# Kernel tuning notes

Measured on AMD Instinct MI355X. Metric: run time of the kernel, lower is better.

## Reference

```python
import jax, jax.numpy as jnp
import numpy as np

B, S, H = 16, 1024, 256
NH = 4
DH = H // NH


def setup_inputs() -> dict:
    key = jax.random.key(0)
    ks = jax.random.split(key, 12)
    w = lambda i, shape: jax.random.normal(ks[i], shape, dtype=jnp.float32) * 0.02
    return {
        "step_sequence": jax.random.normal(ks[0], (B, S, H), dtype=jnp.float32),
        "final_outcomes": jax.random.normal(ks[1], (B,), dtype=jnp.float32),
        "step_mask": jnp.ones((B, S), dtype=jnp.bool_),
        # MultiheadAttention q/k projections (only attn weights are used)
        "Wq": w(2, (H, H)), "bq": jnp.zeros((H,), jnp.float32),
        "Wk": w(3, (H, H)), "bk": jnp.zeros((H,), jnp.float32),
        # causal_mask_predictor: Linear(H,H//2)-ReLU-Linear(H//2,1)-Sigmoid
        "Wm1": w(4, (H, H // 2)), "bm1": jnp.zeros((H // 2,), jnp.float32),
        "Wm2": w(5, (H // 2, 1)), "bm2": jnp.zeros((1,), jnp.float32),
        # intervention_generator: Linear(H,H)-ReLU-Linear(H,H)-Tanh
        "Wi1": w(6, (H, H)), "bi1": jnp.zeros((H,), jnp.float32),
        "Wi2": w(7, (H, H)), "bi2": jnp.zeros((H,), jnp.float32),
        # credit_estimator: Linear(H,H//2)-ReLU-Linear(H//2,1)
        "We1": w(8, (H, H // 2)), "be1": jnp.zeros((H // 2,), jnp.float32),
        "We2": w(9, (H // 2, 1)), "be2": jnp.zeros((1,), jnp.float32),
    }


def _forward(x, final_outcomes, step_mask, Wq, bq, Wk, bk, Wm1, bm1, Wm2, bm2,
             Wi1, bi1, Wi2, bi2, We1, be1, We2, be2):
    # --- CausalAttentionModule ---
    q = (x @ Wq + bq).reshape(B, S, NH, DH).transpose(0, 2, 1, 3)  # [B,NH,S,DH]
    k = (x @ Wk + bk).reshape(B, S, NH, DH).transpose(0, 2, 1, 3)
    scores = jnp.einsum('bhqd,bhkd->bhqk', q, k) / jnp.sqrt(jnp.float32(DH))
    scores = jnp.where(step_mask[:, None, None, :], scores, -jnp.inf)  # key_padding_mask
    attn = jax.nn.softmax(scores, axis=-1).mean(axis=1)  # head-averaged [B,S,S]
    strengths = jax.nn.sigmoid(jax.nn.relu(x @ Wm1 + bm1) @ Wm2 + bm2)[..., 0]  # [B,S]
    aw_mean = attn.mean(axis=1)  # mean over query dim -> [B,S]
    cm = aw_mean[:, None, :] * strengths[:, :, None]  # [B,S,S]
    cm = cm * jnp.tril(jnp.ones((S, S), dtype=x.dtype))[None]
    # --- interventional credit (vectorized over the B x S python loop) ---
    colmean = cm.mean(axis=1)  # mean_i cm[b,i,j] -> [B,S]
    base = (x * colmean[..., None]).mean(axis=1)  # [B,H] baseline weighted-mean feature
    # intervention changes only row t: delta = 0.1*tanh-MLP(x_t)
    delta = 0.1 * jnp.tanh(jax.nn.relu(x @ Wi1 + bi1) @ Wi2 + bi2)  # [B,S,H]
    feats = base[:, None, :] + delta * colmean[..., None] / S  # [B,S,H]
    outcomes = (jax.nn.relu(feats @ We1 + be1) @ We2 + be2)[..., 0]  # [B,S]
    credit = jnp.where(step_mask, final_outcomes[:, None] - outcomes, 0.0)
    return credit, cm


def reference(step_sequence, final_outcomes, step_mask, Wq, bq, Wk, bk,
              Wm1, bm1, Wm2, bm2, Wi1, bi1, Wi2, bi2, We1, be1, We2, be2):
    return _forward(step_sequence, final_outcomes, step_mask, Wq, bq, Wk, bk,
                    Wm1, bm1, Wm2, bm2, Wi1, bi1, Wi2, bi2, We1, be1, We2, be2)
```

## Files before the change

kernel.cpp:

```cpp
#include <hip/hip_runtime.h>
#include <hip/hip_bf16.h>
#include <math.h>

#define B 16
#define S 1024
#define H 256
#define NH 4
#define DH 64
#define BS (B*S)
#define XSTR 264
#define L2E 1.4426950408889634f

typedef short short8 __attribute__((ext_vector_type(8)));
typedef float f32x16 __attribute__((ext_vector_type(16)));

__device__ __forceinline__ unsigned short to_bf16(float v) {
  __hip_bfloat16 h = __float2bfloat16(v);
  return *(unsigned short*)&h;
}
__device__ __forceinline__ unsigned int pack_bf16x2(float a, float b) {
  return (unsigned int)to_bf16(a) | ((unsigned int)to_bf16(b) << 16);
}
__device__ __forceinline__ float exp2_hw(float v) {
  return __builtin_amdgcn_exp2f(v);
}

__global__ __launch_bounds__(256) void k_convert_w(
    const float* __restrict__ Wq, const float* __restrict__ Wk,
    const float* __restrict__ Wm1, const float* __restrict__ Wi1,
    const float* __restrict__ Wi2, const float* __restrict__ We1,
    unsigned short* __restrict__ WqT, unsigned short* __restrict__ WkT,
    unsigned short* __restrict__ Wm1T, unsigned short* __restrict__ Wi1T,
    unsigned short* __restrict__ Wi2T, unsigned short* __restrict__ We1T)
{
  const float* src; unsigned short* dst; int N;
  switch (blockIdx.y) {
    case 0: src = Wq;  dst = WqT;  N = 256; break;
    case 1: src = Wk;  dst = WkT;  N = 256; break;
    case 2: src = Wm1; dst = Wm1T; N = 128; break;
    case 3: src = Wi1; dst = Wi1T; N = 256; break;
    case 4: src = Wi2; dst = Wi2T; N = 256; break;
    default: src = We1; dst = We1T; N = 128; break;
  }
  int ntiles = N >> 5;
  int tile = blockIdx.x;
  if (tile >= 8 * ntiles) return;
  int kt = tile / ntiles, nt = tile % ntiles;
  __shared__ float tl[32][33];
  int t = threadIdx.x, r = t >> 5, c = t & 31;
  #pragma unroll
  for (int i = 0; i < 4; ++i)
    tl[r + i*8][c] = src[(kt*32 + r + i*8)*N + nt*32 + c];
  __syncthreads();
  #pragma unroll
  for (int i = 0; i < 4; ++i)
    dst[(nt*32 + r + i*8)*256 + kt*32 + c] = to_bf16(tl[c][r + i*8]);
}

__global__ __launch_bounds__(256) void k_qkproj_mfma(
    const float* __restrict__ x,
    const unsigned short* __restrict__ WqT, const unsigned short* __restrict__ WkT,
    const float* __restrict__ bq, const float* __restrict__ bk,
    unsigned short* __restrict__ qbuf, unsigned short* __restrict__ kbuf)
{
  __shared__ unsigned short xs[32*XSTR];
  int t = threadIdx.x, wave = t >> 6, lane = t & 63;
  int l5 = lane & 31, h5 = lane >> 5;
  int r0 = blockIdx.x * 32;
  {
    const float4* xg = (const float4*)(x + (size_t)r0*H);
    #pragma unroll
    for (int it = 0; it < 8; ++it) {
      int u = it*256 + t, r = u >> 6, c4 = u & 63;
      float4 v = xg[u];
      uint2 pk; pk.x = pack_bf16x2(v.x, v.y); pk.y = pack_bf16x2(v.z, v.w);
      *(uint2*)&xs[r*XSTR + c4*4] = pk;
    }
  }
  __syncthreads();
  int n0 = wave*64 + l5;
  f32x16 aq0, aq1, ak0, ak1;
  #pragma unroll
  for (int r = 0; r < 16; ++r) { aq0[r]=0.f; aq1[r]=0.f; ak0[r]=0.f; ak1[r]=0.f; }
  #pragma unroll 8
  for (int kc = 0; kc < 16; ++kc) {
    short8 a  = *(const short8*)&xs[l5*XSTR + kc*16 + h5*8];
    short8 q0 = *(const short8*)&WqT[(size_t)n0*256 + kc*16 + h5*8];
    short8 q1 = *(const short8*)&WqT[(size_t)(n0+32)*256 + kc*16 + h5*8];
    short8 k0 = *(const short8*)&WkT[(size_t)n0*256 + kc*16 + h5*8];
    short8 k1 = *(const short8*)&WkT[(size_t)(n0+32)*256 + kc*16 + h5*8];
    aq0 = __builtin_amdgcn_mfma_f32_32x32x16_bf16(a, q0, aq0, 0, 0, 0);
    aq1 = __builtin_amdgcn_mfma_f32_32x32x16_bf16(a, q1, aq1, 0, 0, 0);
    ak0 = __builtin_amdgcn_mfma_f32_32x32x16_bf16(a, k0, ak0, 0, 0, 0);
    ak1 = __builtin_amdgcn_mfma_f32_32x32x16_bf16(a, k1, ak1, 0, 0, 0);
  }
  const float qsc = 0.125f * L2E;
  __syncthreads();
  {
    float b0 = bq[n0], b1 = bq[n0+32];
    #pragma unroll
    for (int r = 0; r < 16; ++r) {
      int row = (r & 3) + 8*(r >> 2) + 4*h5;
      xs[row*XSTR + n0]      = to_bf16((aq0[r] + b0) * qsc);
      xs[row*XSTR + n0 + 32] = to_bf16((aq1[r] + b1) * qsc);
    }
  }
  __syncthreads();
  #pragma unroll
  for (int it = 0; it < 4; ++it) {
    int u = it*256 + t, r = u >> 5, c8 = u & 31;
    int mg = r0 + r, bb = mg >> 10, s = mg & 1023;
    int hh = c8 >> 3, dd = (c8 & 7) * 8;
    *(uint4*)&qbuf[(size_t)(((bb*NH + hh)*S + s)*DH + dd)] = *(uint4*)&xs[r*XSTR + c8*8];
  }
  __syncthreads();
  {
    float b0 = bk[n0], b1 = bk[n0+32];
    #pragma unroll
    for (int r = 0; r < 16; ++r) {
      int row = (r & 3) + 8*(r >> 2) + 4*h5;
      xs[row*XSTR + n0]      = to_bf16(ak0[r] + b0);
      xs[row*XSTR + n0 + 32] = to_bf16(ak1[r] + b1);
    }
  }
  __syncthreads();
  #pragma unroll
  for (int it = 0; it < 4; ++it) {
    int u = it*256 + t, r = u >> 5, c8 = u & 31;
    int mg = r0 + r, bb = mg >> 10, s = mg & 1023;
    int hh = c8 >> 3, dd = (c8 & 7) * 8;
    *(uint4*)&kbuf[(size_t)(((bb*NH + hh)*S + s)*DH + dd)] = *(uint4*)&xs[r*XSTR + c8*8];
  }
}

__global__ __launch_bounds__(256) void k_strengths_mfma(
    const float* __restrict__ x, const unsigned short* __restrict__ Wm1T,
    const float* __restrict__ bm1, const float* __restrict__ Wm2, const float* __restrict__ bm2,
    float* __restrict__ strengths)
{
  __shared__ unsigned short xs[32*XSTR];
  __shared__ float red[4][32];
  int t = threadIdx.x, wave = t >> 6, lane = t & 63;
  int l5 = lane & 31, h5 = lane >> 5;
  int r0 = blockIdx.x * 32;
  {
    const float4* xg = (const float4*)(x + (size_t)r0*H);
    #pragma unroll
    for (int it = 0; it < 8; ++it) {
      int u = it*256 + t, r = u >> 6, c4 = u & 63;
      float4 v = xg[u];
      uint2 pk; pk.x = pack_bf16x2(v.x, v.y); pk.y = pack_bf16x2(v.z, v.w);
      *(uint2*)&xs[r*XSTR + c4*4] = pk;
    }
  }
  __syncthreads();
  f32x16 acc;
  #pragma unroll
  for (int r = 0; r < 16; ++r) acc[r] = 0.f;
  int n = wave*32 + l5;
  #pragma unroll 8
  for (int kc = 0; kc < 16; ++kc) {
    short8 a = *(const short8*)&xs[l5*XSTR + kc*16 + h5*8];
    short8 b = *(const short8*)&Wm1T[(size_t)n*256 + kc*16 + h5*8];
    acc = __builtin_amdgcn_mfma_f32_32x32x16_bf16(a, b, acc, 0, 0, 0);
  }
  float bi = bm1[n], w2 = Wm2[n];
  #pragma unroll
  for (int r = 0; r < 16; ++r) {
    float v = fmaxf(acc[r] + bi, 0.f) * w2;
    #pragma unroll
    for (int off = 1; off <= 16; off <<= 1) v += __shfl_xor(v, off);
    if (l5 == 0) red[wave][(r & 3) + 8*(r >> 2) + 4*h5] = v;
  }
  __syncthreads();
  if (t < 32) {
    float s = red[0][t] + red[1][t] + red[2][t] + red[3][t] + bm2[0];
    strengths[r0 + t] = 1.f / (1.f + __expf(-s));
  }
}

__global__ __launch_bounds__(256) void k_attn_mfma(
    const unsigned short* __restrict__ qbuf, const unsigned short* __restrict__ kbuf,
    float* __restrict__ aw_part)
{
  __shared__ float part[4][64];
  int t = threadIdx.x, wave = t >> 6, lane = t & 63;
  int l5 = lane & 31, h5 = lane >> 5;
  int qt = blockIdx.x, i0 = qt * 64;
  int h = blockIdx.y, b = blockIdx.z;
  const unsigned short* qg = qbuf + (size_t)((b*NH + h)*S + i0) * DH;
  const unsigned short* kg = kbuf + (size_t)((b*NH + h)*S) * DH;

  short8 af[2][4];
  #pragma unroll
  for (int rt = 0; rt < 2; ++rt)
    #pragma unroll
    for (int kc = 0; kc < 4; ++kc)
      af[rt][kc] = *(const short8*)(qg + (rt*32 + l5)*DH + kc*16 + h5*8);

  float lacc[2][16];
  #pragma unroll
  for (int rt = 0; rt < 2; ++rt)
    #pragma unroll
    for (int r = 0; r < 16; ++r) lacc[rt][r] = 0.f;

  unsigned int pp[8][2][8];
  #pragma unroll
  for (int kt = 0; kt < 8; ++kt) {
    short8 bfr[4];
    #pragma unroll
    for (int kc = 0; kc < 4; ++kc)
      bfr[kc] = *(const short8*)(kg + (size_t)(kt*128 + wave*32 + l5)*DH + kc*16 + h5*8);
    f32x16 a0, a1;
    #pragma unroll
    for (int r = 0; r < 16; ++r) { a0[r] = 0.f; a1[r] = 0.f; }
    #pragma unroll
    for (int kc = 0; kc < 4; ++kc) {
      a0 = __builtin_amdgcn_mfma_f32_32x32x16_bf16(af[0][kc], bfr[kc], a0, 0, 0, 0);
      a1 = __builtin_amdgcn_mfma_f32_32x32x16_bf16(af[1][kc], bfr[kc], a1, 0, 0, 0);
    }
    #pragma unroll
    for (int r2 = 0; r2 < 8; ++r2) {
      float p0 = exp2_hw(a0[2*r2]), p1 = exp2_hw(a0[2*r2+1]);
      lacc[0][2*r2] += p0; lacc[0][2*r2+1] += p1;
      pp[kt][0][r2] = pack_bf16x2(p0, p1);
      float q0 = exp2_hw(a1[2*r2]), q1 = exp2_hw(a1[2*r2+1]);
      lacc[1][2*r2] += q0; lacc[1][2*r2+1] += q1;
      pp[kt][1][r2] = pack_bf16x2(q0, q1);
    }
  }
  #pragma unroll
  for (int rt = 0; rt < 2; ++rt)
    #pragma unroll
    for (int r = 0; r < 16; ++r) {
      float v = lacc[rt][r];
      #pragma unroll
      for (int off = 1; off <= 16; off <<= 1) v += __shfl_xor(v, off);
      lacc[rt][r] = v;
    }
  if (l5 == 0) {
    #pragma unroll
    for (int rt = 0; rt < 2; ++rt)
      #pragma unroll
      for (int r = 0; r < 16; ++r)
        part[wave][rt*32 + (r & 3) + 8*(r >> 2) + 4*h5] = lacc[rt][r];
  }
  __syncthreads();
  float linv[2][16];
  #pragma unroll
  for (int rt = 0; rt < 2; ++rt)
    #pragma unroll
    for (int r = 0; r < 16; ++r) {
      int row = rt*32 + (r & 3) + 8*(r >> 2) + 4*h5;
      linv[rt][r] = 1.f / (part[0][row] + part[1][row] + part[2][row] + part[3][row]);
    }
  #pragma unroll
  for (int kt = 0; kt < 8; ++kt) {
    float csum = 0.f;
    #pragma unroll
    for (int rt = 0; rt < 2; ++rt)
      #pragma unroll
      for (int r2 = 0; r2 < 8; ++r2) {
        unsigned int u = pp[kt][rt][r2];
        float p0 = __uint_as_float(u << 16);
        float p1 = __uint_as_float(u & 0xffff0000u);
        csum += p0 * linv[rt][2*r2] + p1 * linv[rt][2*r2+1];
      }
    csum += __shfl_xor(csum, 32);
    if (lane < 32)
      aw_part[(size_t)qt*BS + b*S + kt*128 + wave*32 + lane] = csum;
  }
}

__global__ __launch_bounds__(256) void k_colmean(
    const float* __restrict__ strengths, const float* __restrict__ aw_part,
    float* __restrict__ aw_mean, float* __restrict__ colmean)
{
  __shared__ float st[1024];
  int t = threadIdx.x, b = blockIdx.x;
  #pragma unroll
  for (int e = 0; e < 4; ++e) st[t + e*256] = strengths[b*S + t + e*256];
  __syncthreads();
  for (int off = 1; off < 1024; off <<= 1) {
    float tmp[4];
    #pragma unroll
    for (int e = 0; e < 4; ++e) {
      int j = t + e*256;
      tmp[e] = (j + off < 1024) ? st[j + off] : 0.f;
    }
    __syncthreads();
    #pragma unroll
    for (int e = 0; e < 4; ++e) st[t + e*256] += tmp[e];
    __syncthreads();
  }
  #pragma unroll
  for (int e = 0; e < 4; ++e) {
    int j = t + e*256;
    float s = 0.f;
    #pragma unroll
    for (int qt = 0; qt < 16; ++qt) s += aw_part[(size_t)qt*BS + b*S + j];
    float am = s * (1.f / (NH * (float)S));
    aw_mean[b*S + j] = am;
    colmean[b*S + j] = am * st[j] * (1.f / (float)S);
  }
}

__global__ __launch_bounds__(256) void k_cm(
    const float* __restrict__ aw_mean, const float* __restrict__ strengths,
    float* __restrict__ cm_out)
{
  int t = threadIdx.x;
  int row = blockIdx.x;
  int b = row >> 10, i = row & 1023;
  float sti = strengths[row];
  float4 v = ((const float4*)(aw_mean + b*S))[t];
  int j0 = t * 4;
  float4 o;
  o.x = (j0 + 0 <= i) ? v.x * sti : 0.f;
  o.y = (j0 + 1 <= i) ? v.y * sti : 0.f;
  o.z = (j0 + 2 <= i) ? v.z * sti : 0.f;
  o.w = (j0 + 3 <= i) ? v.w * sti : 0.f;
  ((float4*)cm_out)[(size_t)row*(S/4) + t] = o;
}

__global__ __launch_bounds__(256) void k_base(
    const float* __restrict__ x, const float* __restrict__ colmean,
    float* __restrict__ base_part)
{
  int t = threadIdx.x;
  int chunk = blockIdx.x, b = blockIdx.y;
  float acc = 0.f;
  int t0 = chunk * 32;
  for (int tt = 0; tt < 32; ++tt) {
    int srow = t0 + tt;
    acc += x[(size_t)(b*S + srow)*H + t] * colmean[b*S + srow];
  }
  base_part[(size_t)chunk*B*H + b*H + t] = acc * (1.f / (float)S);
}

__global__ __launch_bounds__(256) void k_credit_mfma(
    const float* __restrict__ x, const float* __restrict__ base_part,
    const float* __restrict__ colmean,
    const unsigned short* __restrict__ Wi1T, const float* __restrict__ bi1,
    const unsigned short* __restrict__ Wi2T, const float* __restrict__ bi2,
    const unsigned short* __restrict__ We1T, const float* __restrict__ be1,
    const float* __restrict__ We2, const float* __restrict__ be2,
    const float* __restrict__ final_outcomes, float* __restrict__ credit_out)
{
  __shared__ unsigned short xs[32*XSTR];
  __shared__ unsigned short hs[32*XSTR];
  __shared__ float cmv_s[32];
  __shared__ float red[4][32];
  int t = threadIdx.x, wave = t >> 6, lane = t & 63;
  int l5 = lane & 31, h5 = lane >> 5;
  int r0 = blockIdx.x * 32;
  int b = r0 >> 10;
  {
    const float4* xg = (const float4*)(x + (size_t)r0*H);
    #pragma unroll
    for (int it = 0; it < 8; ++it) {
      int u = it*256 + t, r = u >> 6, c4 = u & 63;
      float4 v = xg[u];
      uint2 pk; pk.x = pack_bf16x2(v.x, v.y); pk.y = pack_bf16x2(v.z, v.w);
      *(uint2*)&xs[r*XSTR + c4*4] = pk;
    }
  }
  if (t < 32) cmv_s[t] = colmean[r0 + t];
  int n0 = wave*64 + l5;
  float bb0 = 0.f, bb1 = 0.f;
  #pragma unroll
  for (int c = 0; c < 32; ++c) {
    bb0 += base_part[(size_t)c*B*H + b*H + n0];
    bb1 += base_part[(size_t)c*B*H + b*H + n0 + 32];
  }
  __syncthreads();

  {
    f32x16 acc0, acc1;
    #pragma unroll
    for (int r = 0; r < 16; ++r) { acc0[r] = 0.f; acc1[r] = 0.f; }
    #pragma unroll 8
    for (int kc = 0; kc < 16; ++kc) {
      short8 a = *(const short8*)&xs[l5*XSTR + kc*16 + h5*8];
      short8 b0 = *(const short8*)&Wi1T[(size_t)n0*256 + kc*16 + h5*8];
      short8 b1 = *(const short8*)&Wi1T[(size_t)(n0+32)*256 + kc*16 + h5*8];
      acc0 = __builtin_amdgcn_mfma_f32_32x32x16_bf16(a, b0, acc0, 0, 0, 0);
      acc1 = __builtin_amdgcn_mfma_f32_32x32x16_bf16(a, b1, acc1, 0, 0, 0);
    }
    float bi0 = bi1[n0], biv1 = bi1[n0 + 32];
    #pragma unroll
    for (int r = 0; r < 16; ++r) {
      int row = (r & 3) + 8*(r >> 2) + 4*h5;
      hs[row*XSTR + n0]      = to_bf16(fmaxf(acc0[r] + bi0, 0.f));
      hs[row*XSTR + n0 + 32] = to_bf16(fmaxf(acc1[r] + biv1, 0.f));
    }
  }
  __syncthreads();
  {
    f32x16 acc0, acc1;
    #pragma unroll
    for (int r = 0; r < 16; ++r) { acc0[r] = 0.f; acc1[r] = 0.f; }
    #pragma unroll 8
    for (int kc = 0; kc < 16; ++kc) {
      short8 a = *(const short8*)&hs[l5*XSTR + kc*16 + h5*8];
      short8 b0 = *(const short8*)&Wi2T[(size_t)n0*256 + kc*16 + h5*8];
      short8 b1 = *(const short8*)&Wi2T[(size_t)(n0+32)*256 + kc*16 + h5*8];
      acc0 = __builtin_amdgcn_mfma_f32_32x32x16_bf16(a, b0, acc0, 0, 0, 0);
      acc1 = __builtin_amdgcn_mfma_f32_32x32x16_bf16(a, b1, acc1, 0, 0, 0);
    }
    float bi0 = bi2[n0], biv1 = bi2[n0 + 32];
    __syncthreads();
    #pragma unroll
    for (int r = 0; r < 16; ++r) {
      int row = (r & 3) + 8*(r >> 2) + 4*h5;
      float cmv = cmv_s[row] * (0.1f / (float)S);
      float e0 = __expf(2.f*(acc0[r] + bi0));
      float e1 = __expf(2.f*(acc1[r] + biv1));
      float th0 = (e0 - 1.f) / (e0 + 1.f);
      float th1 = (e1 - 1.f) / (e1 + 1.f);
      xs[row*XSTR + n0]      = to_bf16(bb0 + th0 * cmv);
      xs[row*XSTR + n0 + 32] = to_bf16(bb1 + th1 * cmv);
    }
  }
  __syncthreads();
  {
    f32x16 acc;
    #pragma unroll
    for (int r = 0; r < 16; ++r) acc[r] = 0.f;
    int n = wave*32 + l5;
    #pragma unroll 8
    for (int kc = 0; kc < 16; ++kc) {
      short8 a = *(const short8*)&xs[l5*XSTR + kc*16 + h5*8];
      short8 bfrag = *(const short8*)&We1T[(size_t)n*256 + kc*16 + h5*8];
      acc = __builtin_amdgcn_mfma_f32_32x32x16_bf16(a, bfrag, acc, 0, 0, 0);
    }
    float bev = be1[n], w2 = We2[n];
    #pragma unroll
    for (int r = 0; r < 16; ++r) {
      float v = fmaxf(acc[r] + bev, 0.f) * w2;
      #pragma unroll
      for (int off = 1; off <= 16; off <<= 1) v += __shfl_xor(v, off);
      if (l5 == 0) red[wave][(r & 3) + 8*(r >> 2) + 4*h5] = v;
    }
  }
  __syncthreads();
  if (t < 32) {
    float s = red[0][t] + red[1][t] + red[2][t] + red[3][t] + be2[0];
    credit_out[r0 + t] = final_outcomes[b] - s;
  }
}

extern "C" void kernel_launch(void* const* d_in, const int* in_sizes, int n_in,
                              void* d_out, int out_size, void* d_ws, size_t ws_size,
                              hipStream_t stream) {
  (void)in_sizes; (void)n_in; (void)out_size; (void)ws_size;
  const float* x   = (const float*)d_in[0];
  const float* fin = (const float*)d_in[1];
  const float* Wq  = (const float*)d_in[3];  const float* bq  = (const float*)d_in[4];
  const float* Wk  = (const float*)d_in[5];  const float* bk  = (const float*)d_in[6];
  const float* Wm1 = (const float*)d_in[7];  const float* bm1 = (const float*)d_in[8];
  const float* Wm2 = (const float*)d_in[9];  const float* bm2 = (const float*)d_in[10];
  const float* Wi1 = (const float*)d_in[11]; const float* bi1 = (const float*)d_in[12];
  const float* Wi2 = (const float*)d_in[13]; const float* bi2 = (const float*)d_in[14];
  const float* We1 = (const float*)d_in[15]; const float* be1 = (const float*)d_in[16];
  const float* We2 = (const float*)d_in[17]; const float* be2 = (const float*)d_in[18];

  unsigned short* us = (unsigned short*)d_ws;
  unsigned short* qb   = us;
  unsigned short* kb   = qb + (size_t)B*NH*S*DH;
  unsigned short* WqT  = kb + (size_t)B*NH*S*DH;
  unsigned short* WkT  = WqT + 65536;
  unsigned short* Wi1T = WkT + 65536;
  unsigned short* Wi2T = Wi1T + 65536;
  unsigned short* Wm1T = Wi2T + 65536;
  unsigned short* We1T = Wm1T + 32768;
  float* fs = (float*)(We1T + 32768);
  float* aw_part   = fs;
  float* strengths = aw_part + 16*BS;
  float* aw_mean   = strengths + BS;
  float* colmean   = aw_mean + BS;
  float* base_part = colmean + BS;

  float* credit_out = (float*)d_out;
  float* cm_out     = credit_out + BS;

  k_convert_w     <<<dim3(64, 6), 256, 0, stream>>>(Wq, Wk, Wm1, Wi1, Wi2, We1,
                                                    WqT, WkT, Wm1T, Wi1T, Wi2T, We1T);
  k_qkproj_mfma   <<<BS/32, 256, 0, stream>>>(x, WqT, WkT, bq, bk, qb, kb);
  k_strengths_mfma<<<BS/32, 256, 0, stream>>>(x, Wm1T, bm1, Wm2, bm2, strengths);
  k_attn_mfma     <<<dim3(S/64, NH, B), 256, 0, stream>>>(qb, kb, aw_part);
  k_colmean       <<<B, 256, 0, stream>>>(strengths, aw_part, aw_mean, colmean);
  k_base          <<<dim3(32, B), 256, 0, stream>>>(x, colmean, base_part);
  k_cm            <<<BS, 256, 0, stream>>>(aw_mean, strengths, cm_out);
  k_credit_mfma   <<<BS/32, 256, 0, stream>>>(x, base_part, colmean, Wi1T, bi1, Wi2T, bi2,
                                              We1T, be1, We2, be2, fin, credit_out);
}
```

Measured before the change: 233.1 us.

## Recompute attention scores in a second pass instead of caching probabilities in registers

The attention kernel now handles 32 query rows per block instead of 64. Rather than keeping every exp-score in a large packed-bf16 register array, it makes two passes over the keys. The first pass accumulates row sums, and the second recomputes QK^T and normalizes with exp2(score - log2(sum)). This frees many registers to raise occupancy and doubles the grid, at the cost of twice the MFMA and K loads. The per-tile partial buffer also doubles, so colmean now sums 32 partials.

After: 250.1 us. 7.3% more time.

```diff
diff --git a/kernel.cpp b/kernel.cpp
--- a/kernel.cpp
+++ b/kernel.cpp
@@ -23,6 +23,9 @@
 }
 __device__ __forceinline__ float exp2_hw(float v) {
   return __builtin_amdgcn_exp2f(v);
+}
+__device__ __forceinline__ float log2_hw(float v) {
+  return __builtin_amdgcn_logf(v);
 }
 
 __global__ __launch_bounds__(256) void k_convert_w(
@@ -183,92 +186,73 @@
     const unsigned short* __restrict__ qbuf, const unsigned short* __restrict__ kbuf,
     float* __restrict__ aw_part)
 {
-  __shared__ float part[4][64];
+  __shared__ float part[4][32];
   int t = threadIdx.x, wave = t >> 6, lane = t & 63;
   int l5 = lane & 31, h5 = lane >> 5;
-  int qt = blockIdx.x, i0 = qt * 64;
+  int qt = blockIdx.x, i0 = qt * 32;
   int h = blockIdx.y, b = blockIdx.z;
   const unsigned short* qg = qbuf + (size_t)((b*NH + h)*S + i0) * DH;
   const unsigned short* kg = kbuf + (size_t)((b*NH + h)*S) * DH;
 
-  short8 af[2][4];
-  #pragma unroll
-  for (int rt = 0; rt < 2; ++rt)
-    #pragma unroll
-    for (int kc = 0; kc < 4; ++kc)
-      af[rt][kc] = *(const short8*)(qg + (rt*32 + l5)*DH + kc*16 + h5*8);
-
-  float lacc[2][16];
-  #pragma unroll
-  for (int rt = 0; rt < 2; ++rt)
-    #pragma unroll
-    for (int r = 0; r < 16; ++r) lacc[rt][r] = 0.f;
-
-  unsigned int pp[8][2][8];
-  #pragma unroll
+  short8 af[4];
+  #pragma unroll
+  for (int kc = 0; kc < 4; ++kc)
+    af[kc] = *(const short8*)(qg + l5*DH + kc*16 + h5*8);
+
+  float lacc[16];
+  #pragma unroll
+  for (int r = 0; r < 16; ++r) lacc[r] = 0.f;
+
   for (int kt = 0; kt < 8; ++kt) {
     short8 bfr[4];
     #pragma unroll
     for (int kc = 0; kc < 4; ++kc)
       bfr[kc] = *(const short8*)(kg + (size_t)(kt*128 + wave*32 + l5)*DH + kc*16 + h5*8);
-    f32x16 a0, a1;
-    #pragma unroll
-    for (int r = 0; r < 16; ++r) { a0[r] = 0.f; a1[r] = 0.f; }
-    #pragma unroll
-    for (int kc = 0; kc < 4; ++kc) {
-      a0 = __builtin_amdgcn_mfma_f32_32x32x16_bf16(af[0][kc], bfr[kc], a0, 0, 0, 0);
-      a1 = __builtin_amdgcn_mfma_f32_32x32x16_bf16(af[1][kc], bfr[kc], a1, 0, 0, 0);
-    }
-    #pragma unroll
-    for (int r2 = 0; r2 < 8; ++r2) {
-      float p0 = exp2_hw(a0[2*r2]), p1 = exp2_hw(a0[2*r2+1]);
-      lacc[0][2*r2] += p0; lacc[0][2*r2+1] += p1;
-      pp[kt][0][r2] = pack_bf16x2(p0, p1);
-      float q0 = exp2_hw(a1[2*r2]), q1 = exp2_hw(a1[2*r2+1]);
-      lacc[1][2*r2] += q0; lacc[1][2*r2+1] += q1;
-      pp[kt][1][r2] = pack_bf16x2(q0, q1);
-    }
-  }
-  #pragma unroll
-  for (int rt = 0; rt < 2; ++rt)
-    #pragma unroll
-    for (int r = 0; r < 16; ++r) {
-      float v = lacc[rt][r];
-      #pragma unroll
-      for (int off = 1; off <= 16; off <<= 1) v += __shfl_xor(v, off);
-      lacc[rt][r] = v;
-    }
+    f32x16 acc;
+    #pragma unroll
+    for (int r = 0; r < 16; ++r) acc[r] = 0.f;
+    #pragma unroll
+    for (int kc = 0; kc < 4; ++kc)
+      acc = __builtin_amdgcn_mfma_f32_32x32x16_bf16(af[kc], bfr[kc], acc, 0, 0, 0);
+    #pragma unroll
+    for (int r = 0; r < 16; ++r) lacc[r] += exp2_hw(acc[r]);
+  }
+  #pragma unroll
+  for (int r = 0; r < 16; ++r) {
+    float v = lacc[r];
+    #pragma unroll
+    for (int off = 1; off <= 16; off <<= 1) v += __shfl_xor(v, off);
+    lacc[r] = v;
+  }
   if (l5 == 0) {
     #pragma unroll
-    for (int rt = 0; rt < 2; ++rt)
-      #pragma unroll
-      for (int r = 0; r < 16; ++r)
-        part[wave][rt*32 + (r & 3) + 8*(r >> 2) + 4*h5] = lacc[rt][r];
-  }
-  __syncthreads();
-  float linv[2][16];
-  #pragma unroll
-  for (int rt = 0; rt < 2; ++rt)
-    #pragma unroll
-    for (int r = 0; r < 16; ++r) {
-      int row = rt*32 + (r & 3) + 8*(r >> 2) + 4*h5;
-      linv[rt][r] = 1.f / (part[0][row] + part[1][row] + part[2][row] + part[3][row]);
-    }
-  #pragma unroll
+    for (int r = 0; r < 16; ++r)
+      part[wave][(r & 3) + 8*(r >> 2) + 4*h5] = lacc[r];
+  }
+  __syncthreads();
+  float llog[16];
+  #pragma unroll
+  for (int r = 0; r < 16; ++r) {
+    int row = (r & 3) + 8*(r >> 2) + 4*h5;
+    llog[r] = log2_hw(part[0][row] + part[1][row] + part[2][row] + part[3][row]);
+  }
   for (int kt = 0; kt < 8; ++kt) {
+    short8 bfr[4];
+    #pragma unroll
+    for (int kc = 0; kc < 4; ++kc)
+      bfr[kc] = *(const short8*)(kg + (size_t)(kt*128 + wave*32 + l5)*DH + kc*16 + h5*8);
+    f32x16 acc;
+    #pragma unroll
+    for (int r = 0; r < 16; ++r) acc[r] = 0.f;
+    #pragma unroll
+    for (int kc = 0; kc < 4; ++kc)
+      acc = __builtin_amdgcn_mfma_f32_32x32x16_bf16(af[kc], bfr[kc], acc, 0, 0, 0);
     float csum = 0.f;
     #pragma unroll
-    for (int rt = 0; rt < 2; ++rt)
-      #pragma unroll
-      for (int r2 = 0; r2 < 8; ++r2) {
-        unsigned int u = pp[kt][rt][r2];
-        float p0 = __uint_as_float(u << 16);
-        float p1 = __uint_as_float(u & 0xffff0000u);
-        csum += p0 * linv[rt][2*r2] + p1 * linv[rt][2*r2+1];
-      }
+    for (int r = 0; r < 16; ++r) csum += exp2_hw(acc[r] - llog[r]);
     csum += __shfl_xor(csum, 32);
     if (lane < 32)
-      aw_part[(size_t)qt*BS + b*S + kt*128 + wave*32 + lane] = csum;
+      aw_part[(size_t)qt*BS + b*S + kt*128 + wave*32 + l5] = csum;
   }
 }
 
@@ -298,7 +282,7 @@
     int j = t + e*256;
     float s = 0.f;
     #pragma unroll
-    for (int qt = 0; qt < 16; ++qt) s += aw_part[(size_t)qt*BS + b*S + j];
+    for (int qt = 0; qt < 32; ++qt) s += aw_part[(size_t)qt*BS + b*S + j];
     float am = s * (1.f / (NH * (float)S));
     aw_mean[b*S + j] = am;
     colmean[b*S + j] = am * st[j] * (1.f / (float)S);
@@ -476,7 +460,7 @@
   unsigned short* We1T = Wm1T + 32768;
   float* fs = (float*)(We1T + 32768);
   float* aw_part   = fs;
-  float* strengths = aw_part + 16*BS;
+  float* strengths = aw_part + 32*BS;
   float* aw_mean   = strengths + BS;
   float* colmean   = aw_mean + BS;
   float* base_part = colmean + BS;
@@ -488,7 +472,7 @@
                                                     WqT, WkT, Wm1T, Wi1T, Wi2T, We1T);
   k_qkproj_mfma   <<<BS/32, 256, 0, stream>>>(x, WqT, WkT, bq, bk, qb, kb);
   k_strengths_mfma<<<BS/32, 256, 0, stream>>>(x, Wm1T, bm1, Wm2, bm2, strengths);
-  k_attn_mfma     <<<dim3(S/64, NH, B), 256, 0, stream>>>(qb, kb, aw_part);
+  k_attn_mfma     <<<dim3(S/32, NH, B), 256, 0, stream>>>(qb, kb, aw_part);
   k_colmean       <<<B, 256, 0, stream>>>(strengths, aw_part, aw_mean, colmean);
   k_base          <<<dim3(32, B), 256, 0, stream>>>(x, colmean, base_part);
   k_cm            <<<BS, 256, 0, stream>>>(aw_mean, strengths, cm_out);
```
